# Performance work log

Hardware: AMD Instinct MI355X
Metric: run time of the kernel (lower is better)

## Reference

```python
import jax, jax.numpy as jnp
import numpy as np
from jax import lax

B, L_ENC, L_DEC = 16, 2048, 1024
ENC_IN, MARK_IN, C_OUT = 7, 4, 7
D_MODEL, N_HEADS, D_FF = 512, 8, 2048
E_LAYERS, D_LAYERS, FACTOR, PRED_LEN = 3, 2, 5, 512


def _pos_embed(L, d):
    pos = np.arange(L, dtype=np.float32)[:, None]
    div = np.exp(np.arange(0, d, 2, dtype=np.float32) * -(np.log(10000.0) / d))
    pe = np.zeros((L, d), np.float32)
    pe[:, 0::2] = np.sin(pos * div)
    pe[:, 1::2] = np.cos(pos * div)
    return jnp.asarray(pe)


def _layer_norm(x, g, b, eps=1e-5):
    m = jnp.mean(x, -1, keepdims=True)
    v = jnp.mean((x - m) ** 2, -1, keepdims=True)
    return (x - m) * lax.rsqrt(v + eps) * g + b


def _circ_conv1d(x, w):
    # x:[B,L,Cin], w:[Cout,Cin,3], circular padding=1 (TokenEmbedding / ConvLayer)
    xp = jnp.concatenate([x[:, -1:], x, x[:, :1]], axis=1)
    y = lax.conv_general_dilated(xp.transpose(0, 2, 1), w, (1,), 'VALID',
                                 dimension_numbers=('NCH', 'OIH', 'NCH'))
    return y.transpose(0, 2, 1)


def _prob_attention(q, k, v, mask_flag, rng):
    # q,k,v: [B,L,H,Dh] -> [B,H,L,Dh]
    q, k, v = (t.transpose(0, 2, 1, 3) for t in (q, k, v))
    Bq, H, Lq, Dh = q.shape
    Lk = k.shape[2]
    U_part = min(FACTOR * int(np.ceil(np.log(Lk))), Lk)  # sampled keys per query
    u = min(FACTOR * int(np.ceil(np.log(Lq))), Lq)       # top queries kept
    idx = jax.random.randint(rng, (Lq, U_part), 0, Lk)
    k_sample = k[:, :, idx, :]                           # [B,H,Lq,U,Dh]
    qk_sample = jnp.einsum('bhld,bhlsd->bhls', q, k_sample)
    M = qk_sample.max(-1) - qk_sample.sum(-1) / Lk       # sparsity measure
    _, m_top = lax.top_k(M, u)                            # [B,H,u]
    q_red = jnp.take_along_axis(q, m_top[..., None], axis=2)
    scores = jnp.einsum('bhud,bhkd->bhuk', q_red, k) / np.sqrt(Dh).astype(np.float32)
    if mask_flag:
        tri = jnp.triu(jnp.ones((Lq, Lk), bool), 1)
        scores = jnp.where(tri[m_top], -jnp.inf, scores)  # ProbMask
        ctx = jnp.cumsum(v, axis=2)                       # masked initial context
    else:
        ctx = jnp.broadcast_to(jnp.mean(v, 2, keepdims=True), (Bq, H, Lq, Dh))
    attn = jax.nn.softmax(scores, -1)
    upd = jnp.einsum('bhuk,bhkd->bhud', attn, v)
    bi = jnp.arange(Bq)[:, None, None]
    hi = jnp.arange(H)[None, :, None]
    ctx = ctx.at[bi, hi, m_top].set(upd)                  # scatter top-u contexts
    return ctx.transpose(0, 2, 1, 3)


def _attn_layer(xq, xkv, w, b, mask_flag, rng):
    Bq, Lq, d = xq.shape
    Dh = d // N_HEADS
    q = (xq @ w[0] + b[0]).reshape(Bq, Lq, N_HEADS, Dh)
    k = (xkv @ w[1] + b[1]).reshape(Bq, -1, N_HEADS, Dh)
    v = (xkv @ w[2] + b[2]).reshape(Bq, -1, N_HEADS, Dh)
    out = _prob_attention(q, k, v, mask_flag, rng).reshape(Bq, Lq, d)
    return out @ w[3] + b[3]


def _ffn(x, w1, b1, w2, b2):
    # Conv1d kernel-size-1 pair == pointwise MLP
    return jax.nn.gelu(x @ w1 + b1, approximate=False) @ w2 + b2


def _distil(x, cw, cb, bg, bb):
    y = _circ_conv1d(x, cw) + cb
    y = y * (bg / np.sqrt(1.0 + 1e-5).astype(np.float32)) + bb  # BN eval (mean0,var1)
    y = jax.nn.elu(y)
    y = y.transpose(0, 2, 1)
    y = lax.reduce_window(y, -jnp.inf, lax.max, (1, 1, 3), (1, 1, 2),
                          [(0, 0), (0, 0), (1, 1)])  # MaxPool1d(k=3,s=2,p=1)
    return y.transpose(0, 2, 1)


def setup_inputs() -> dict:
    key = jax.random.key(0)
    ks = iter(jax.random.split(key, 64))
    rn = lambda shape: jax.random.normal(next(ks), shape, jnp.float32) * 0.02
    return {
        'x_enc': jax.random.normal(next(ks), (B, L_ENC, ENC_IN), jnp.float32),
        'x_mark_enc': jax.random.normal(next(ks), (B, L_ENC, MARK_IN), jnp.float32),
        'x_dec': jax.random.normal(next(ks), (B, L_DEC, ENC_IN), jnp.float32),
        'x_mark_dec': jax.random.normal(next(ks), (B, L_DEC, MARK_IN), jnp.float32),
        'enc_tok_w': rn((D_MODEL, ENC_IN, 3)),
        'enc_mark_w': rn((MARK_IN, D_MODEL)),
        'dec_tok_w': rn((D_MODEL, ENC_IN, 3)),
        'dec_mark_w': rn((MARK_IN, D_MODEL)),
        'enc_attn_w': rn((E_LAYERS, 4, D_MODEL, D_MODEL)),
        'enc_attn_b': jnp.zeros((E_LAYERS, 4, D_MODEL), jnp.float32),
        'enc_ffn1_w': rn((E_LAYERS, D_MODEL, D_FF)),
        'enc_ffn1_b': jnp.zeros((E_LAYERS, D_FF), jnp.float32),
        'enc_ffn2_w': rn((E_LAYERS, D_FF, D_MODEL)),
        'enc_ffn2_b': jnp.zeros((E_LAYERS, D_MODEL), jnp.float32),
        'enc_ln_g': jnp.ones((E_LAYERS, 2, D_MODEL), jnp.float32),
        'enc_ln_b': jnp.zeros((E_LAYERS, 2, D_MODEL), jnp.float32),
        'distil_w': rn((E_LAYERS - 1, D_MODEL, D_MODEL, 3)),
        'distil_b': jnp.zeros((E_LAYERS - 1, D_MODEL), jnp.float32),
        'distil_bn_g': jnp.ones((E_LAYERS - 1, D_MODEL), jnp.float32),
        'distil_bn_b': jnp.zeros((E_LAYERS - 1, D_MODEL), jnp.float32),
        'enc_norm_g': jnp.ones((D_MODEL,), jnp.float32),
        'enc_norm_b': jnp.zeros((D_MODEL,), jnp.float32),
        'dec_self_w': rn((D_LAYERS, 4, D_MODEL, D_MODEL)),
        'dec_self_b': jnp.zeros((D_LAYERS, 4, D_MODEL), jnp.float32),
        'dec_cross_w': rn((D_LAYERS, 4, D_MODEL, D_MODEL)),
        'dec_cross_b': jnp.zeros((D_LAYERS, 4, D_MODEL), jnp.float32),
        'dec_ffn1_w': rn((D_LAYERS, D_MODEL, D_FF)),
        'dec_ffn1_b': jnp.zeros((D_LAYERS, D_FF), jnp.float32),
        'dec_ffn2_w': rn((D_LAYERS, D_FF, D_MODEL)),
        'dec_ffn2_b': jnp.zeros((D_LAYERS, D_MODEL), jnp.float32),
        'dec_ln_g': jnp.ones((D_LAYERS, 3, D_MODEL), jnp.float32),
        'dec_ln_b': jnp.zeros((D_LAYERS, 3, D_MODEL), jnp.float32),
        'dec_norm_g': jnp.ones((D_MODEL,), jnp.float32),
        'dec_norm_b': jnp.zeros((D_MODEL,), jnp.float32),
        'proj_w': rn((D_MODEL, C_OUT)),
        'proj_b': jnp.zeros((C_OUT,), jnp.float32),
    }


def reference(x_enc, x_mark_enc, x_dec, x_mark_dec, enc_tok_w, enc_mark_w,
              dec_tok_w, dec_mark_w, enc_attn_w, enc_attn_b, enc_ffn1_w, enc_ffn1_b,
              enc_ffn2_w, enc_ffn2_b, enc_ln_g, enc_ln_b, distil_w, distil_b,
              distil_bn_g, distil_bn_b, enc_norm_g, enc_norm_b, dec_self_w, dec_self_b,
              dec_cross_w, dec_cross_b, dec_ffn1_w, dec_ffn1_b, dec_ffn2_w, dec_ffn2_b,
              dec_ln_g, dec_ln_b, dec_norm_g, dec_norm_b, proj_w, proj_b):
    base = jax.random.key(42)
    # DataEmbedding: token conv + sinusoid positional + time-feature linear
    x = _circ_conv1d(x_enc, enc_tok_w) + _pos_embed(x_enc.shape[1], D_MODEL)[None] + x_mark_enc @ enc_mark_w
    for l in range(E_LAYERS):
        h = x + _attn_layer(x, x, enc_attn_w[l], enc_attn_b[l], False, jax.random.fold_in(base, l))
        h = _layer_norm(h, enc_ln_g[l, 0], enc_ln_b[l, 0])
        y = _ffn(h, enc_ffn1_w[l], enc_ffn1_b[l], enc_ffn2_w[l], enc_ffn2_b[l])
        x = _layer_norm(h + y, enc_ln_g[l, 1], enc_ln_b[l, 1])
        if l < E_LAYERS - 1:  # distil conv halves the length
            x = _distil(x, distil_w[l], distil_b[l], distil_bn_g[l], distil_bn_b[l])
    enc_out = _layer_norm(x, enc_norm_g, enc_norm_b)
    x = _circ_conv1d(x_dec, dec_tok_w) + _pos_embed(x_dec.shape[1], D_MODEL)[None] + x_mark_dec @ dec_mark_w
    for l in range(D_LAYERS):
        h = x + _attn_layer(x, x, dec_self_w[l], dec_self_b[l], True, jax.random.fold_in(base, 100 + 2 * l))
        h = _layer_norm(h, dec_ln_g[l, 0], dec_ln_b[l, 0])
        h = h + _attn_layer(h, enc_out, dec_cross_w[l], dec_cross_b[l], False, jax.random.fold_in(base, 101 + 2 * l))
        h = _layer_norm(h, dec_ln_g[l, 1], dec_ln_b[l, 1])
        y = _ffn(h, dec_ffn1_w[l], dec_ffn1_b[l], dec_ffn2_w[l], dec_ffn2_b[l])
        x = _layer_norm(h + y, dec_ln_g[l, 2], dec_ln_b[l, 2])
    x = _layer_norm(x, dec_norm_g, dec_norm_b)
    out = x @ proj_w + proj_b
    return out[:, -PRED_LEN:, :]
```

## Files before the change

kernel.cpp:

```cpp
#include <hip/hip_runtime.h>
#include <math.h>
#include <stdint.h>

typedef unsigned int u32;
typedef _Float16 f16;
typedef __attribute__((ext_vector_type(8))) _Float16 f16x8;
typedef __attribute__((ext_vector_type(4))) float f32x4;

__host__ __device__ __forceinline__ u32 rotl32(u32 x, int r) { return (x << r) | (x >> (32 - r)); }
__host__ __device__ __forceinline__ void tf_round(u32& x0, u32& x1, int r) {
  x0 += x1; x1 = rotl32(x1, r); x1 ^= x0;
}
__host__ __device__ __forceinline__ void tf_block(u32 k0, u32 k1, u32 x0, u32 x1, u32& o0, u32& o1) {
  u32 k2 = k0 ^ k1 ^ 0x1BD11BDAu;
  x0 += k0; x1 += k1;
  tf_round(x0,x1,13); tf_round(x0,x1,15); tf_round(x0,x1,26); tf_round(x0,x1,6);
  x0 += k1; x1 += k2 + 1u;
  tf_round(x0,x1,17); tf_round(x0,x1,29); tf_round(x0,x1,16); tf_round(x0,x1,24);
  x0 += k2; x1 += k0 + 2u;
  tf_round(x0,x1,13); tf_round(x0,x1,15); tf_round(x0,x1,26); tf_round(x0,x1,6);
  x0 += k0; x1 += k1 + 3u;
  tf_round(x0,x1,17); tf_round(x0,x1,29); tf_round(x0,x1,16); tf_round(x0,x1,24);
  x0 += k1; x1 += k2 + 4u;
  tf_round(x0,x1,13); tf_round(x0,x1,15); tf_round(x0,x1,26); tf_round(x0,x1,6);
  x0 += k2; x1 += k0 + 5u;
  o0 = x0; o1 = x1;
}

__global__ void k_idx(u32 ka, u32 kb, int n, int mask, int* __restrict__ idx) {
  int i = blockIdx.x * 256 + threadIdx.x;
  if (i >= n) return;
  u32 b1, b2; tf_block(ka, kb, 0u, (u32)i, b1, b2);
  idx[i] = (int)((b1 ^ b2) & (u32)mask);
}

__device__ __forceinline__ void emit_split(float v, f16* __restrict__ oh,
                                           f16* __restrict__ ol, size_t o) {
  f16 h = (f16)v;
  oh[o] = h;
  ol[o] = (f16)((v - (float)h) * 2048.0f);
}
__device__ __forceinline__ float rsplit(const f16* __restrict__ h,
                                        const f16* __restrict__ l, size_t o) {
  return (float)h[o] + (float)l[o] * (1.0f / 2048.0f);
}

__global__ void k_pe(float* __restrict__ pe) {
  int i = blockIdx.x * 256 + threadIdx.x;
  if (i >= 2048 * 512) return;
  int t = i >> 9, o = i & 511;
  float arg = (float)((o >> 1) * 2) * (float)(-(log(10000.0) / 512.0));
  float div = (float)exp((double)arg);
  float ang32 = (float)t * div;
  double ang = (double)ang32;
  pe[i] = (float)((o & 1) ? cos(ang) : sin(ang));
}

__global__ __launch_bounds__(256) void k_embed(
    const float* __restrict__ x, const float* __restrict__ mark,
    const float* __restrict__ tw, const float* __restrict__ mw,
    const float* __restrict__ pe, f16* __restrict__ oh, f16* __restrict__ ol,
    int L, int total) {
  int i = blockIdx.x * 256 + threadIdx.x;
  if (i >= total) return;
  int oo = i & 511;
  int bt = i >> 9;
  int t = bt % L;
  int b = bt / L;
  float acc = pe[(t << 9) + oo];
  #pragma unroll
  for (int k = 0; k < 3; ++k) {
    int st = t + k - 1; if (st < 0) st += L; else if (st >= L) st -= L;
    const float* xr = x + (size_t)(b * L + st) * 7;
    const float* wr = tw + oo * 21 + k;
    #pragma unroll
    for (int ii = 0; ii < 7; ++ii) acc += xr[ii] * wr[ii * 3];
  }
  const float* mr = mark + (size_t)bt * 4;
  #pragma unroll
  for (int m = 0; m < 4; ++m) acc += mr[m] * mw[(m << 9) + oo];
  emit_split(acc, oh, ol, ((size_t)bt << 9) + oo);
}

__global__ __launch_bounds__(256) void k_wsplit(const float* __restrict__ W,
    f16* __restrict__ Wh, f16* __restrict__ Wl, int K, int N) {
  size_t zo = (size_t)blockIdx.z * K * N;
  W += zo; Wh += zo; Wl += zo;
  __shared__ float tile[32][33];
  int kb = blockIdx.x << 5, nb = blockIdx.y << 5;
  int t = threadIdx.x;
  int tr = t >> 5, tc = t & 31;
  #pragma unroll
  for (int p = 0; p < 4; ++p)
    tile[tr + p * 8][tc] = W[(size_t)(kb + tr + p * 8) * N + nb + tc];
  __syncthreads();
  #pragma unroll
  for (int p = 0; p < 4; ++p) {
    int n = tr + p * 8, k = tc;
    float v = tile[k][n];
    f16 h = (f16)v;
    size_t o = (size_t)(nb + n) * K + kb + k;
    Wh[o] = h;
    Wl[o] = (f16)((v - (float)h) * 2048.0f);
  }
}

__global__ void k_wsplit_conv(const float* __restrict__ w, f16* __restrict__ Wh, f16* __restrict__ Wl) {
  int i = blockIdx.x * 256 + threadIdx.x;
  if (i >= 512 * 1536) return;
  int o = i / 1536, k = i - o * 1536;
  float v = w[(size_t)o * 1536 + (k & 511) * 3 + (k >> 9)];
  f16 h = (f16)v;
  Wh[i] = h;
  Wl[i] = (f16)((v - (float)h) * 2048.0f);
}

__device__ __forceinline__ int swz_x(int r) { return ((((r >> 1) & 3) ^ ((r >> 3) & 3)) << 4); }

__device__ __forceinline__ void gload16(const void* g, void* l) {
  __builtin_amdgcn_global_load_lds(
      (const __attribute__((address_space(1))) void*)g,
      (__attribute__((address_space(3))) void*)l, 16, 0, 0);
}

template<int ACT, int OSPLIT, int GATHER, int RESID>
__global__ __launch_bounds__(256, 2) void k_mgemm2(
    const f16* __restrict__ Ah, const f16* __restrict__ Al,
    const f16* __restrict__ Bh, const f16* __restrict__ Bl,
    const float* __restrict__ bias,
    const f16* __restrict__ Rh, const f16* __restrict__ Rl,
    const float* __restrict__ bns, const float* __restrict__ bnb,
    float* __restrict__ C, f16* __restrict__ Ch, f16* __restrict__ Cl,
    int M, int N, int K, int lgL) {
  __shared__ char lds[65536];
  const int t = threadIdx.x;
  int nwg = gridDim.x * gridDim.y;
  int bid = blockIdx.y * gridDim.x + blockIdx.x;
  if ((nwg & 7) == 0) {
    int cpx = nwg >> 3;
    bid = (bid & 7) * cpx + (bid >> 3);
  }
  const int bm = (bid / gridDim.x) << 7, bn = (bid % gridDim.x) << 7;
  const int w = t >> 6, l = t & 63;
  const int lr = l >> 2;
  const int qx = (l & 3) << 4;
  const int wr = (w >> 1) << 6, wc = (w & 1) << 6;
  const int fr = l & 15;
  const int fkB = (l >> 4) << 4;
  const f32x4 zero = {0.f, 0.f, 0.f, 0.f};
  f32x4 acc1[4][4], acc2[4][4];
  #pragma unroll
  for (int i = 0; i < 4; ++i)
    #pragma unroll
    for (int j = 0; j < 4; ++j) { acc1[i][j] = zero; acc2[i][j] = zero; }

  auto stage = [&](int k0, int bufo) {
    #pragma unroll
    for (int c = 0; c < 2; ++c) {
      int r = w * 32 + c * 16 + lr;
      int sx = qx ^ swz_x(r);
      const char *gAh, *gAl;
      if (GATHER) {
        int m = bm + r;
        int Lm = 1 << lgL;
        int ab = m >> lgL, at = m & (Lm - 1);
        int ke = k0 + (sx >> 1);
        int tap = ke >> 9, ii = ke & 511;
        int st = at + tap - 1; if (st < 0) st += Lm; else if (st >= Lm) st -= Lm;
        size_t aoff = (((size_t)((ab << lgL) + st)) << 9) + ii;
        gAh = (const char*)(Ah + aoff);
        gAl = (const char*)(Al + aoff);
      } else {
        gAh = (const char*)(Ah + (size_t)(bm + r) * K + k0) + sx;
        gAl = (const char*)(Al + (size_t)(bm + r) * K + k0) + sx;
      }
      const char* gBh = (const char*)(Bh + (size_t)(bn + r) * K + k0) + sx;
      const char* gBl = (const char*)(Bl + (size_t)(bn + r) * K + k0) + sx;
      char* base = lds + bufo + w * 2048 + c * 1024;
      gload16(gAh, base);
      gload16(gAl, base + 8192);
      gload16(gBh, base + 16384);
      gload16(gBl, base + 24576);
    }
  };

  int nt = K >> 5;
  stage(0, 0);
  __syncthreads();
  int bufo = 0;
  for (int tt = 0; tt < nt; ++tt) {
    int nb = bufo ^ 32768;
    if (tt + 1 < nt) stage((tt + 1) << 5, nb);
    char* pAh = lds + bufo;
    char* pAl = pAh + 8192;
    char* pBh = pAh + 16384;
    char* pBl = pAh + 24576;
    f16x8 ah4[4], al4[4];
    #pragma unroll
    for (int i = 0; i < 4; ++i) {
      int r = wr + i * 16 + fr;
      int ob = r * 64 + (fkB ^ swz_x(r));
      ah4[i] = *(f16x8*)(pAh + ob);
      al4[i] = *(f16x8*)(pAl + ob);
    }
    #pragma unroll
    for (int j = 0; j < 4; ++j) {
      int r = wc + j * 16 + fr;
      int ob = r * 64 + (fkB ^ swz_x(r));
      f16x8 bh_ = *(f16x8*)(pBh + ob);
      f16x8 bl_ = *(f16x8*)(pBl + ob);
      #pragma unroll
      for (int i = 0; i < 4; ++i) {
        acc1[i][j] = __builtin_amdgcn_mfma_f32_16x16x32_f16(ah4[i], bh_, acc1[i][j], 0, 0, 0);
        acc2[i][j] = __builtin_amdgcn_mfma_f32_16x16x32_f16(ah4[i], bl_, acc2[i][j], 0, 0, 0);
        acc2[i][j] = __builtin_amdgcn_mfma_f32_16x16x32_f16(al4[i], bh_, acc2[i][j], 0, 0, 0);
      }
    }
    __syncthreads();
    bufo = nb;
  }
  #pragma unroll
  for (int j = 0; j < 4; ++j) {
    int col = bn + wc + j * 16 + fr;
    float bsv = bias[col];
    float g2 = 0.f, b2 = 0.f;
    if (ACT == 2) { g2 = bns[col] * 0.9999950000375f; b2 = bnb[col]; }
    #pragma unroll
    for (int i = 0; i < 4; ++i) {
      #pragma unroll
      for (int r = 0; r < 4; ++r) {
        int row = bm + wr + i * 16 + ((l >> 4) << 2) + r;
        float v = acc1[i][j][r] + acc2[i][j][r] * (1.0f / 2048.0f) + bsv;
        if (ACT == 1) v = 0.5f * v * (1.0f + erff(v * 0.70710678118654752f));
        if (ACT == 2) { v = v * g2 + b2; v = v > 0.f ? v : expm1f(v); }
        size_t oi = (size_t)row * N + col;
        if (RESID) v += rsplit(Rh, Rl, oi);
        if (OSPLIT) emit_split(v, Ch, Cl, oi);
        else        C[oi] = v;
      }
    }
  }
}

__global__ __launch_bounds__(256) void k_ln(const f16* __restrict__ xh, const f16* __restrict__ xl,
    const float* __restrict__ g, const float* __restrict__ b,
    float* __restrict__ of32, f16* __restrict__ oh, f16* __restrict__ ol) {
  int row = blockIdx.x, t = threadIdx.x;
  size_t base = (size_t)row << 9;
  float v0 = rsplit(xh, xl, base + t);
  float v1 = rsplit(xh, xl, base + t + 256);
  float s = v0 + v1;
  #pragma unroll
  for (int off = 32; off; off >>= 1) s += __shfl_down(s, off);
  __shared__ float ls[4];
  if ((t & 63) == 0) ls[t >> 6] = s;
  __syncthreads();
  float mean = (ls[0] + ls[1] + ls[2] + ls[3]) * (1.f / 512.f);
  __syncthreads();
  float d0 = v0 - mean, d1 = v1 - mean;
  float q = d0 * d0 + d1 * d1;
  #pragma unroll
  for (int off = 32; off; off >>= 1) q += __shfl_down(q, off);
  if ((t & 63) == 0) ls[t >> 6] = q;
  __syncthreads();
  float var = (ls[0] + ls[1] + ls[2] + ls[3]) * (1.f / 512.f);
  float rs = rsqrtf(var + 1e-5f);
  float r0 = d0 * rs * g[t] + b[t];
  float r1 = d1 * rs * g[t + 256] + b[t + 256];
  if (of32) { of32[base + t] = r0; of32[base + t + 256] = r1; }
  if (oh) {
    emit_split(r0, oh, ol, base + t);
    emit_split(r1, oh, ol, base + t + 256);
  }
}

__global__ __launch_bounds__(256) void k_qkM(const float* __restrict__ Q, int qstr,
    const float* __restrict__ Kp, int kstr, const int* __restrict__ idx,
    float* __restrict__ M, int Lq, int Lk, int U) {
  __shared__ float qsh[4][2][64];
  __shared__ int idxs[4][2][40];
  int nwg = gridDim.x;
  int bid = blockIdx.x;
  if ((nwg & 7) == 0) {
    int cpx = nwg >> 3;
    bid = (bid & 7) * cpx + (bid >> 3);
  }
  int wib = threadIdx.x >> 6;
  int wid = (bid << 2) + wib;
  int lane = threadIdx.x & 63;
  int Lh = Lq >> 1;
  int lp = wid & (Lh - 1);
  int bh = wid / Lh;
  int l0 = lp * 2;
  int h = bh & 7; int b = bh >> 3;
  if (lane < 32) {
    int q = lane >> 4, e = lane & 15;
    const float4* qr = (const float4*)(Q + (size_t)(b * Lq + l0 + q) * qstr + (h << 6));
    *(float4*)(&qsh[wib][q][e * 4]) = qr[e];
  }
  if (lane < U) {
    idxs[wib][0][lane] = idx[l0 * U + lane];
    idxs[wib][1][lane] = idx[(l0 + 1) * U + lane];
  }
  __syncthreads();
  int g = lane >> 2, j = lane & 3;
  float mx0 = -INFINITY, sm0 = 0.f, mx1 = -INFINITY, sm1 = 0.f;
  #pragma unroll
  for (int p = 0; p < 5; ++p) {
    int sp = p * 16 + g;
    int q = (sp >= U) ? 1 : 0;
    int s = sp - U * q;
    bool act = sp < 2 * U;
    int kr = idxs[wib][act ? q : 0][act ? s : 0];
    const float* kb_ = Kp + (size_t)((size_t)b * Lk + kr) * kstr + (h << 6);
    float4 c0 = *(const float4*)(kb_ +  0 + 4 * j);
    float4 c1 = *(const float4*)(kb_ + 16 + 4 * j);
    float4 c2 = *(const float4*)(kb_ + 32 + 4 * j);
    float4 c3 = *(const float4*)(kb_ + 48 + 4 * j);
    const float* qs = qsh[wib][act ? q : 0];
    float pd = 0.f;
    pd += qs[ 0 + 4*j] * c0.x + qs[ 1 + 4*j] * c0.y + qs[ 2 + 4*j] * c0.z + qs[ 3 + 4*j] * c0.w;
    pd += qs[16 + 4*j] * c1.x + qs[17 + 4*j] * c1.y + qs[18 + 4*j] * c1.z + qs[19 + 4*j] * c1.w;
    pd += qs[32 + 4*j] * c2.x + qs[33 + 4*j] * c2.y + qs[34 + 4*j] * c2.z + qs[35 + 4*j] * c2.w;
    pd += qs[48 + 4*j] * c3.x + qs[49 + 4*j] * c3.y + qs[50 + 4*j] * c3.z + qs[51 + 4*j] * c3.w;
    pd += __shfl_xor(pd, 1);
    pd += __shfl_xor(pd, 2);
    if (act) {
      if (q == 0) { mx0 = fmaxf(mx0, pd); sm0 += pd; }
      else        { mx1 = fmaxf(mx1, pd); sm1 += pd; }
    }
  }
  #pragma unroll
  for (int off = 32; off >= 4; off >>= 1) {
    mx0 = fmaxf(mx0, __shfl_xor(mx0, off)); sm0 += __shfl_xor(sm0, off);
    mx1 = fmaxf(mx1, __shfl_xor(mx1, off)); sm1 += __shfl_xor(sm1, off);
  }
  if (lane == 0) {
    M[(size_t)bh * Lq + l0]     = mx0 - sm0 / (float)Lk;
    M[(size_t)bh * Lq + l0 + 1] = mx1 - sm1 / (float)Lk;
  }
}

__global__ void k_topk64(const float* __restrict__ M, int* __restrict__ mtop, int Lq, int u) {
  __shared__ float vals[2048];
  int bh = blockIdx.x, l = threadIdx.x;
  const float* Mr = M + (size_t)bh * Lq;
  for (int i = l; i < Lq; i += 64) vals[i] = Mr[i];
  __syncthreads();
  for (int it = 0; it < u; ++it) {
    float bv = -INFINITY; int bi = 0x7fffffff;
    for (int i = l; i < Lq; i += 64) {
      float v = vals[i];
      if (v > bv || (v == bv && i < bi)) { bv = v; bi = i; }
    }
    #pragma unroll
    for (int off = 32; off; off >>= 1) {
      float vv = __shfl_xor(bv, off); int ii = __shfl_xor(bi, off);
      if (vv > bv || (vv == bv && ii < bi)) { bv = vv; bi = ii; }
    }
    if (l == 0) { mtop[bh * u + it] = bi; vals[bi] = -INFINITY; }
    __syncthreads();
  }
}

__global__ void k_cm1(const float* __restrict__ V, int vstr, float* __restrict__ PS,
                      int Lk, int rows) {
  int bid = blockIdx.x;
  int bh = bid >> 4, seg = bid & 15, d = threadIdx.x;
  int b = bh >> 3, h = bh & 7;
  const float* vp = V + (size_t)(b * Lk + seg * rows) * vstr + (h << 6) + d;
  float acc = 0.f;
  for (int r = 0; r < rows; ++r) acc += vp[(size_t)r * vstr];
  PS[(bid << 6) + d] = acc;
}
__global__ void k_cm2(const float* __restrict__ PS, f16* __restrict__ AOh,
                      f16* __restrict__ AOl, float invLk, int Lq, int total) {
  int i = blockIdx.x * 256 + threadIdx.x;
  if (i >= total) return;
  int c = i & 511; int h = c >> 6; int d = c & 63;
  int r = i >> 9; int b = r / Lq;
  float acc = 0.f;
  #pragma unroll
  for (int s = 0; s < 16; ++s) acc += PS[(((((b << 3) + h) << 4) + s) << 6) + d];
  emit_split(acc * invLk, AOh, AOl, (size_t)i);
}

__global__ void k_cs1(const float* __restrict__ V, int vstr, float* __restrict__ PS,
                      int Lq, int rows) {
  int bid = blockIdx.x;
  int bh = bid >> 3, seg = bid & 7, d = threadIdx.x;
  int b = bh >> 3, h = bh & 7;
  const float* vp = V + (size_t)(b * Lq + seg * rows) * vstr + (h << 6) + d;
  float acc = 0.f;
  for (int r = 0; r < rows; ++r) acc += vp[(size_t)r * vstr];
  PS[(bid << 6) + d] = acc;
}
__global__ void k_cs3(const float* __restrict__ V, int vstr, const float* __restrict__ PS,
                      f16* __restrict__ AOh, f16* __restrict__ AOl, int Lq, int rows) {
  int bid = blockIdx.x;
  int bh = bid >> 3, seg = bid & 7, d = threadIdx.x;
  int b = bh >> 3, h = bh & 7;
  float acc = 0.f;
  for (int s2 = 0; s2 < seg; ++s2) acc += PS[(((bh << 3) + s2) << 6) + d];
  const float* vp = V + (size_t)(b * Lq + seg * rows) * vstr + (h << 6) + d;
  size_t ob = ((size_t)(b * Lq + seg * rows) << 9) + (h << 6) + d;
  for (int r = 0; r < rows; ++r) {
    acc += vp[(size_t)r * vstr];
    emit_split(acc, AOh, AOl, ob + ((size_t)r << 9));
  }
}

__global__ __launch_bounds__(256) void k_sattnF(
    const float* __restrict__ Q, int qstr, const float* __restrict__ Kp, int kstr,
    const float* __restrict__ Vp, int vstr, const int* __restrict__ mtop,
    float* __restrict__ PPm, float* __restrict__ PPs, float* __restrict__ PPv,
    int Lq, int Lk, int u, int masked, int bhn, int chunk) {
  __shared__ float Qs[40 * 64];
  __shared__ float Kt[64 * 65];
  __shared__ float Vs[64 * 65];
  __shared__ float els[40 * 64];
  __shared__ int rowsh[40];
  int ch = blockIdx.x, bh = blockIdx.y;
  int b = bh >> 3, h = bh & 7;
  int c0 = ch * chunk;
  int nkt = chunk >> 6;
  int t = threadIdx.x;
  int g = t >> 6, d = t & 63;
  if (t < 40) rowsh[t] = (t < u) ? mtop[bh * u + t] : -1;
  __syncthreads();
  for (int i = t; i < 40 * 16; i += 256) {
    int r = i >> 4, e4 = i & 15;
    int row = rowsh[r];
    float4 v;
    if (row >= 0) v = *(const float4*)(Q + (size_t)(b * Lq + row) * qstr + (h << 6) + e4 * 4);
    else          v = make_float4(0.f, 0.f, 0.f, 0.f);
    *(float4*)(Qs + r * 64 + e4 * 4) = v;
  }
  int rows_[10];
  __syncthreads();
  #pragma unroll
  for (int i = 0; i < 10; ++i) rows_[i] = rowsh[g + i * 4];
  float pv[10], m[10], sum[10];
  #pragma unroll
  for (int i = 0; i < 10; ++i) { pv[i] = 0.f; m[i] = -INFINITY; sum[i] = 0.f; }
  const int srow = t >> 2, seg = t & 3;
  for (int kt = 0; kt < nkt; ++kt) {
    __syncthreads();
    {
      int crow = c0 + (kt << 6) + srow;
      const float* kp2 = Kp + (size_t)(b * Lk + crow) * kstr + (h << 6) + seg * 16;
      const float* vp2 = Vp + (size_t)(b * Lk + crow) * vstr + (h << 6) + seg * 16;
      #pragma unroll
      for (int q4 = 0; q4 < 4; ++q4) {
        float4 kv = *(const float4*)(kp2 + q4 * 4);
        float4 vv = *(const float4*)(vp2 + q4 * 4);
        int e0 = seg * 16 + q4 * 4;
        Kt[(e0 + 0) * 65 + srow] = kv.x;
        Kt[(e0 + 1) * 65 + srow] = kv.y;
        Kt[(e0 + 2) * 65 + srow] = kv.z;
        Kt[(e0 + 3) * 65 + srow] = kv.w;
        Vs[srow * 65 + e0 + 0] = vv.x;
        Vs[srow * 65 + e0 + 1] = vv.y;
        Vs[srow * 65 + e0 + 2] = vv.z;
        Vs[srow * 65 + e0 + 3] = vv.w;
      }
    }
    __syncthreads();
    float dot[10];
    #pragma unroll
    for (int i = 0; i < 10; ++i) dot[i] = 0.f;
    for (int e = 0; e < 64; ++e) {
      float kv = Kt[e * 65 + d];
      #pragma unroll
      for (int i = 0; i < 10; ++i)
        dot[i] += Qs[(g + i * 4) * 64 + e] * kv;
    }
    int key = c0 + (kt << 6) + d;
    float scale_[10];
    #pragma unroll
    for (int i = 0; i < 10; ++i) {
      float s = dot[i] * 0.125f;
      if (masked && key > rows_[i]) s = -INFINITY;
      float tm = s;
      #pragma unroll
      for (int off = 32; off; off >>= 1) tm = fmaxf(tm, __shfl_xor(tm, off));
      float nm = fmaxf(m[i], tm);
      if (nm > -3e38f) {
        float scl = expf(m[i] - nm);
        float e_ = expf(s - nm);
        float ts = e_;
        #pragma unroll
        for (int off = 32; off; off >>= 1) ts += __shfl_xor(ts, off);
        sum[i] = sum[i] * scl + ts;
        m[i] = nm;
        scale_[i] = scl;
        els[(g + i * 4) * 64 + d] = e_;
      } else {
        scale_[i] = 1.f;
        els[(g + i * 4) * 64 + d] = 0.f;
      }
    }
    __syncthreads();
    float acc[10];
    #pragma unroll
    for (int i = 0; i < 10; ++i) acc[i] = 0.f;
    for (int k = 0; k < 64; ++k) {
      float vv = Vs[k * 65 + d];
      #pragma unroll
      for (int i = 0; i < 10; ++i)
        acc[i] += els[(g + i * 4) * 64 + k] * vv;
    }
    #pragma unroll
    for (int i = 0; i < 10; ++i) pv[i] = pv[i] * scale_[i] + acc[i];
  }
  #pragma unroll
  for (int i = 0; i < 10; ++i) {
    int r = g + i * 4;
    if (r < u) {
      size_t pidx = (size_t)(ch * bhn + bh) * u + r;
      if (d == 0) { PPm[pidx] = m[i]; PPs[pidx] = sum[i]; }
      PPv[pidx * 64 + d] = pv[i];
    }
  }
}

__global__ void k_sattnc(const float* __restrict__ PPm, const float* __restrict__ PPs,
                         const float* __restrict__ PPv, const int* __restrict__ mtop,
                         f16* __restrict__ AOh, f16* __restrict__ AOl,
                         int Lq, int u, int nch, int bhn) {
  int rowid = blockIdx.x;
  int bh = rowid / u, ui = rowid % u;
  int d = threadIdx.x;
  int b = bh >> 3, h = bh & 7;
  int row = mtop[bh * u + ui];
  float M = -INFINITY;
  for (int c = 0; c < nch; ++c)
    M = fmaxf(M, PPm[(size_t)(c * bhn + bh) * u + ui]);
  float S = 0.f, o = 0.f;
  for (int c = 0; c < nch; ++c) {
    size_t pidx = (size_t)(c * bhn + bh) * u + ui;
    float pm = PPm[pidx];
    float sc = (pm > -3e38f) ? expf(pm - M) : 0.f;
    S += sc * PPs[pidx];
    o += sc * PPv[pidx * 64 + d];
  }
  emit_split(o / S, AOh, AOl, ((size_t)(b * Lq + row) << 9) + (h << 6) + d);
}

__global__ void k_maxpool(const float* __restrict__ y, f16* __restrict__ oh,
                          f16* __restrict__ ol, int L) {
  int Lo = L >> 1;
  int i = blockIdx.x * 256 + threadIdx.x;
  int c = i & 511; int bj = i >> 9;
  int j = bj % Lo; int b = bj / Lo;
  float m = -INFINITY;
  int t0 = 2 * j - 1;
  #pragma unroll
  for (int k = 0; k < 3; ++k) {
    int tt = t0 + k;
    if (tt >= 0 && tt < L) m = fmaxf(m, y[((size_t)(b * L + tt) << 9) + c]);
  }
  emit_split(m, oh, ol, ((size_t)(b * Lo + j) << 9) + c);
}

__global__ void k_proj(const float* __restrict__ Xn, const float* __restrict__ pw,
                       const float* __restrict__ pb, float* __restrict__ out) {
  int i = blockIdx.x * 256 + threadIdx.x;
  if (i >= 16 * 512 * 7) return;
  int c = i % 7; int r = i / 7;
  int b = r >> 9; int j = r & 511;
  const float* xr = Xn + ((size_t)(b * 1024 + 512 + j) << 9);
  float acc = pb[c];
  for (int d2 = 0; d2 < 512; ++d2) acc += xr[d2] * pw[d2 * 7 + c];
  out[i] = acc;
}

extern "C" void kernel_launch(void* const* d_in, const int* in_sizes, int n_in,
                              void* d_out, int out_size, void* d_ws, size_t ws_size,
                              hipStream_t stream) {
  const float* x_enc      = (const float*)d_in[0];
  const float* x_mark_enc = (const float*)d_in[1];
  const float* x_dec      = (const float*)d_in[2];
  const float* x_mark_dec = (const float*)d_in[3];
  const float* enc_tok_w  = (const float*)d_in[4];
  const float* enc_mark_w = (const float*)d_in[5];
  const float* dec_tok_w  = (const float*)d_in[6];
  const float* dec_mark_w = (const float*)d_in[7];
  const float* enc_attn_w = (const float*)d_in[8];
  const float* enc_attn_b = (const float*)d_in[9];
  const float* enc_ffn1_w = (const float*)d_in[10];
  const float* enc_ffn1_b = (const float*)d_in[11];
  const float* enc_ffn2_w = (const float*)d_in[12];
  const float* enc_ffn2_b = (const float*)d_in[13];
  const float* enc_ln_g   = (const float*)d_in[14];
  const float* enc_ln_b   = (const float*)d_in[15];
  const float* distil_w   = (const float*)d_in[16];
  const float* distil_b   = (const float*)d_in[17];
  const float* distil_bn_g= (const float*)d_in[18];
  const float* distil_bn_b= (const float*)d_in[19];
  const float* enc_norm_g = (const float*)d_in[20];
  const float* enc_norm_b = (const float*)d_in[21];
  const float* dec_self_w = (const float*)d_in[22];
  const float* dec_self_b = (const float*)d_in[23];
  const float* dec_cross_w= (const float*)d_in[24];
  const float* dec_cross_b= (const float*)d_in[25];
  const float* dec_ffn1_w = (const float*)d_in[26];
  const float* dec_ffn1_b = (const float*)d_in[27];
  const float* dec_ffn2_w = (const float*)d_in[28];
  const float* dec_ffn2_b = (const float*)d_in[29];
  const float* dec_ln_g   = (const float*)d_in[30];
  const float* dec_ln_b   = (const float*)d_in[31];
  const float* dec_norm_g = (const float*)d_in[32];
  const float* dec_norm_b = (const float*)d_in[33];
  const float* proj_w     = (const float*)d_in[34];
  const float* proj_b     = (const float*)d_in[35];

  float* ws = (float*)d_ws;
  size_t off = 0;
  f16* Xh   = (f16*)(ws + off); off += 16777216;
  f16* Xl   = Xh + 16777216;
  f16* ENCh = (f16*)(ws + off); off += 4194304;
  f16* ENCl = ENCh + 4194304;
  float* PE = ws + off; off += 1048576;
  float* Mb = ws + off; off += 131072;
  float* PS = ws + off; off += 65536;
  f16* WSP  = (f16*)(ws + off); off += 2097152;
  int* IDXi = (int*)(ws + off); off += 84480;
  float* Y  = ws + off;
  int* MTi  = IDXi + 81920;
  size_t need4 = (off + 16777216ull) * 4;
  size_t need8 = (off + 33554432ull) * 4;
  int bs;
  if      (ws_size >= need8) bs = 8;
  else if (ws_size >= need4) bs = 4;
  else return;
  f16* Yh = (f16*)Y;
  f16* Yl = Yh + 16777216;
  float* WF  = (float*)WSP + 1048576;
  float* PPm = WF;
  float* PPs = WF + 16384;
  float* PPv = WF + 32768;

  auto ln = [&](const f16* xh, const f16* xl, const float* g, const float* b, int rows,
                float* of32, f16* oh, f16* ol) {
    k_ln<<<rows, 256, 0, stream>>>(xh, xl, g, b, of32, oh, ol);
  };
  auto wsplit = [&](const float* W, f16* Wh, f16* Wl, int K, int N, int nmat) {
    dim3 g(K >> 5, N >> 5, nmat);
    k_wsplit<<<g, 256, 0, stream>>>(W, Wh, Wl, K, N);
  };
  auto mgQ = [&](const f16* Ah, const f16* Al, const f16* Wh, const f16* Wl,
                 const float* bias, float* C, int M, int N, int K) {
    dim3 g(N >> 7, M >> 7);
    k_mgemm2<0,0,0,0><<<g, 256, 0, stream>>>(Ah, Al, Wh, Wl, bias, nullptr, nullptr,
        nullptr, nullptr, C, nullptr, nullptr, M, N, K, 0);
  };
  auto mgR = [&](const f16* Ah, const f16* Al, const f16* Wh, const f16* Wl,
                 const float* bias, const f16* Rh, const f16* Rl,
                 f16* Ch, f16* Cl, int M, int N, int K) {
    dim3 g(N >> 7, M >> 7);
    k_mgemm2<0,1,0,1><<<g, 256, 0, stream>>>(Ah, Al, Wh, Wl, bias, Rh, Rl,
        nullptr, nullptr, nullptr, Ch, Cl, M, N, K, 0);
  };
  auto mgG = [&](const f16* Ah, const f16* Al, const f16* Wh, const f16* Wl,
                 const float* bias, f16* Ch, f16* Cl, int M, int N, int K) {
    dim3 g(N >> 7, M >> 7);
    k_mgemm2<1,1,0,0><<<g, 256, 0, stream>>>(Ah, Al, Wh, Wl, bias, nullptr, nullptr,
        nullptr, nullptr, nullptr, Ch, Cl, M, N, K, 0);
  };
  auto Uof = [](int Lx) { int v = 5 * (int)ceil(log((double)Lx)); return v < Lx ? v : Lx; };

  auto attn = [&](f16* xqh, f16* xql, const f16* xkvh, const f16* xkvl,
                  int Lq, int Lk, const float* w, const float* bias,
                  bool masked, u32 fold, bool selfa) {
    int U = Uof(Lk), uu = Uof(Lq);
    u32 r0, r1, ka, kb2;
    tf_block(0u, 42u, 0u, fold, r0, r1);
    tf_block(r0, r1, 0u, 1u, ka, kb2);
    int n = Lq * U;
    k_idx<<<(n + 255) / 256, 256, 0, stream>>>(ka, kb2, n, Lk - 1, IDXi);

    f16 *Wqkvh = WSP,            *Wqkvl = WSP + 786432;
    f16 *WQh   = WSP,            *WQl   = WSP + 262144;
    f16 *WKVh  = WSP + 524288,   *WKVl  = WSP + 1048576;
    f16 *WOh   = WSP + 1572864,  *WOl   = WSP + 1835008;
    if (selfa) {
      wsplit(w, Wqkvh, Wqkvl, 512, 512, 3);
    } else {
      wsplit(w, WQh, WQl, 512, 512, 1);
      wsplit(w + 262144, WKVh, WKVl, 512, 512, 2);
    }
    wsplit(w + 786432, WOh, WOl, 512, 512, 1);

    int nsl = 16 / bs;
    int bhn = bs * 8;
    for (int s = 0; s < nsl; ++s) {
      size_t qoff = (size_t)s * bs * Lq * 512;
      size_t koff = (size_t)s * bs * Lk * 512;
      const float *qp, *kp, *vp;
      int qstr, kstr, vstr;
      f16 *AOh, *AOl;
      if (selfa) {
        float* QKV = Y;
        AOh = (f16*)(Y + (size_t)bs * Lq * 1536);
        AOl = AOh + (size_t)bs * Lq * 512;
        mgQ(xqh + qoff, xql + qoff, Wqkvh, Wqkvl, bias, QKV, bs * Lq, 1536, 512);
        qp = QKV; qstr = 1536; kp = QKV + 512; kstr = 1536; vp = QKV + 1024; vstr = 1536;
      } else {
        float* Qb  = Y;
        float* KVb = Y + (size_t)bs * Lq * 512;
        AOh = (f16*)(KVb + (size_t)bs * Lk * 1024);
        AOl = AOh + (size_t)bs * Lq * 512;
        mgQ(xqh + qoff, xql + qoff, WQh, WQl, bias, Qb, bs * Lq, 512, 512);
        mgQ(xkvh + koff, xkvl + koff, WKVh, WKVl, bias + 512, KVb, bs * Lk, 1024, 512);
        qp = Qb; qstr = 512; kp = KVb; kstr = 1024; vp = KVb + 512; vstr = 1024;
      }
      int wids = bhn * Lq;
      k_qkM<<<wids / 8, 256, 0, stream>>>(qp, qstr, kp, kstr, IDXi, Mb, Lq, Lk, U);
      k_topk64<<<bhn, 64, 0, stream>>>(Mb, MTi, Lq, uu);
      if (masked) {
        k_cs1<<<bhn * 8, 64, 0, stream>>>(vp, vstr, PS, Lq, Lq >> 3);
        k_cs3<<<bhn * 8, 64, 0, stream>>>(vp, vstr, PS, AOh, AOl, Lq, Lq >> 3);
      } else {
        k_cm1<<<bhn * 16, 64, 0, stream>>>(vp, vstr, PS, Lk, Lk >> 4);
        int tot = bs * Lq * 512;
        k_cm2<<<tot / 256, 256, 0, stream>>>(PS, AOh, AOl, 1.0f / (float)Lk, Lq, tot);
      }
      int chunk = (Lk >= 2048) ? 512 : ((Lk >= 1024) ? 256 : 128);
      int nch = Lk / chunk;
      dim3 gs(nch, bhn);
      k_sattnF<<<gs, 256, 0, stream>>>(qp, qstr, kp, kstr, vp, vstr, MTi,
                                       PPm, PPs, PPv, Lq, Lk, uu, masked ? 1 : 0, bhn, chunk);
      k_sattnc<<<bhn * uu, 64, 0, stream>>>(PPm, PPs, PPv, MTi, AOh, AOl, Lq, uu, nch, bhn);
      mgR(AOh, AOl, WOh, WOl, bias + 1536, xqh + qoff, xql + qoff,
          xqh + qoff, xql + qoff, bs * Lq, 512, 512);
    }
  };

  auto ffn = [&](f16* xh, f16* xl, const float* w1, const float* b1,
                 const float* w2, const float* b2, int Mtot) {
    f16 *W1h = WSP,           *W1l = WSP + 1048576,
        *W2h = WSP + 2097152, *W2l = WSP + 3145728;
    wsplit(w1, W1h, W1l, 512, 2048, 1);
    wsplit(w2, W2h, W2l, 2048, 512, 1);
    for (int c0 = 0; c0 < Mtot; c0 += 8192) {
      int rows = (Mtot - c0 < 8192) ? (Mtot - c0) : 8192;
      mgG(xh + (size_t)c0 * 512, xl + (size_t)c0 * 512, W1h, W1l, b1, Yh, Yl, rows, 2048, 512);
      mgR(Yh, Yl, W2h, W2l, b2, xh + (size_t)c0 * 512, xl + (size_t)c0 * 512,
          xh + (size_t)c0 * 512, xl + (size_t)c0 * 512, rows, 512, 2048);
    }
  };

  k_pe<<<(2048 * 512) / 256, 256, 0, stream>>>(PE);
  k_embed<<<(16 * 2048 * 512) / 256, 256, 0, stream>>>(x_enc, x_mark_enc, enc_tok_w, enc_mark_w,
                                                       PE, Xh, Xl, 2048, 16 * 2048 * 512);
  int L = 2048;
  for (int l = 0; l < 3; ++l) {
    attn(Xh, Xl, Xh, Xl, L, L, enc_attn_w + (size_t)l * 4 * 262144,
         enc_attn_b + (size_t)l * 2048, false, (u32)l, true);
    ln(Xh, Xl, enc_ln_g + (size_t)(l * 2) * 512, enc_ln_b + (size_t)(l * 2) * 512, 16 * L,
       nullptr, Xh, Xl);
    ffn(Xh, Xl, enc_ffn1_w + (size_t)l * 512 * 2048, enc_ffn1_b + (size_t)l * 2048,
        enc_ffn2_w + (size_t)l * 2048 * 512, enc_ffn2_b + (size_t)l * 512, 16 * L);
    ln(Xh, Xl, enc_ln_g + (size_t)(l * 2 + 1) * 512, enc_ln_b + (size_t)(l * 2 + 1) * 512, 16 * L,
       nullptr, Xh, Xl);
    if (l < 2) {
      f16 *Dh = WSP, *Dl = WSP + 786432;
      k_wsplit_conv<<<(512 * 1536) / 256, 256, 0, stream>>>(distil_w + (size_t)l * 512 * 512 * 3, Dh, Dl);
      dim3 g(512 >> 7, (16 * L) >> 7);
      int lgL = (L == 2048) ? 11 : 10;
      k_mgemm2<2,0,1,0><<<g, 256, 0, stream>>>(Xh, Xl, Dh, Dl, distil_b + (size_t)l * 512,
          nullptr, nullptr, distil_bn_g + (size_t)l * 512, distil_bn_b + (size_t)l * 512,
          Y, nullptr, nullptr, 16 * L, 512, 1536, lgL);
      int Lo = L >> 1;
      k_maxpool<<<(16 * Lo * 512) / 256, 256, 0, stream>>>(Y, Xh, Xl, L);
      L = Lo;
    }
  }
  ln(Xh, Xl, enc_norm_g, enc_norm_b, 16 * 512, nullptr, ENCh, ENCl);

  k_embed<<<(16 * 1024 * 512) / 256, 256, 0, stream>>>(x_dec, x_mark_dec, dec_tok_w, dec_mark_w,
                                                       PE, Xh, Xl, 1024, 16 * 1024 * 512);
  for (int l = 0; l < 2; ++l) {
    attn(Xh, Xl, Xh, Xl, 1024, 1024, dec_self_w + (size_t)l * 4 * 262144,
         dec_self_b + (size_t)l * 2048, true, (u32)(100 + 2 * l), true);
    ln(Xh, Xl, dec_ln_g + (size_t)(l * 3) * 512, dec_ln_b + (size_t)(l * 3) * 512, 16384,
       nullptr, Xh, Xl);
    attn(Xh, Xl, ENCh, ENCl, 1024, 512, dec_cross_w + (size_t)l * 4 * 262144,
         dec_cross_b + (size_t)l * 2048, false, (u32)(101 + 2 * l), false);
    ln(Xh, Xl, dec_ln_g + (size_t)(l * 3 + 1) * 512, dec_ln_b + (size_t)(l * 3 + 1) * 512, 16384,
       nullptr, Xh, Xl);
    ffn(Xh, Xl, dec_ffn1_w + (size_t)l * 512 * 2048, dec_ffn1_b + (size_t)l * 2048,
        dec_ffn2_w + (size_t)l * 2048 * 512, dec_ffn2_b + (size_t)l * 512, 16384);
    ln(Xh, Xl, dec_ln_g + (size_t)(l * 3 + 2) * 512, dec_ln_b + (size_t)(l * 3 + 2) * 512, 16384,
       nullptr, Xh, Xl);
  }
  ln(Xh, Xl, dec_norm_g, dec_norm_b, 16384, Y, nullptr, nullptr);
  k_proj<<<(16 * 512 * 7 + 255) / 256, 256, 0, stream>>>(Y, proj_w, proj_b, (float*)d_out);
}
```

Measured before the change: 6.163 ms.

## Process four queries per wave in qkM, widen cumsum split, merge weight splits, larger FFN chunk

The sparsity-measure kernel now has each wavefront handle four query rows instead of two, which halves the grid and reuses the index and Q staging. The masked cumulative-sum kernels split each head into 16 segments instead of 8 for more parallelism. The four attention weight splits are merged into a single wsplit launch. The FFN row chunk doubles to 16384 when the batch slice is 8, to cut launch count. The trade-offs are a dynamic loop with more branching in qkM and a larger FFN intermediate buffer that must fit in the workspace.

```diff
diff --git a/kernel.cpp b/kernel.cpp
--- a/kernel.cpp
+++ b/kernel.cpp
@@ -277,8 +277,8 @@
 __global__ __launch_bounds__(256) void k_qkM(const float* __restrict__ Q, int qstr,
     const float* __restrict__ Kp, int kstr, const int* __restrict__ idx,
     float* __restrict__ M, int Lq, int Lk, int U) {
-  __shared__ float qsh[4][2][64];
-  __shared__ int idxs[4][2][40];
+  __shared__ float qsh[4][4][64];
+  __shared__ int idxs[4][4][40];
   int nwg = gridDim.x;
   int bid = blockIdx.x;
   if ((nwg & 7) == 0) {
@@ -288,36 +288,38 @@
   int wib = threadIdx.x >> 6;
   int wid = (bid << 2) + wib;
   int lane = threadIdx.x & 63;
-  int Lh = Lq >> 1;
+  int Lh = Lq >> 2;
   int lp = wid & (Lh - 1);
   int bh = wid / Lh;
-  int l0 = lp * 2;
+  int l0 = lp * 4;
   int h = bh & 7; int b = bh >> 3;
-  if (lane < 32) {
+  {
     int q = lane >> 4, e = lane & 15;
     const float4* qr = (const float4*)(Q + (size_t)(b * Lq + l0 + q) * qstr + (h << 6));
     *(float4*)(&qsh[wib][q][e * 4]) = qr[e];
   }
   if (lane < U) {
-    idxs[wib][0][lane] = idx[l0 * U + lane];
-    idxs[wib][1][lane] = idx[(l0 + 1) * U + lane];
+    #pragma unroll
+    for (int q = 0; q < 4; ++q)
+      idxs[wib][q][lane] = idx[(l0 + q) * U + lane];
   }
   __syncthreads();
   int g = lane >> 2, j = lane & 3;
   float mx0 = -INFINITY, sm0 = 0.f, mx1 = -INFINITY, sm1 = 0.f;
-  #pragma unroll
-  for (int p = 0; p < 5; ++p) {
+  float mx2 = -INFINITY, sm2 = 0.f, mx3 = -INFINITY, sm3 = 0.f;
+  int npass = (4 * U + 15) >> 4;
+  for (int p = 0; p < npass; ++p) {
     int sp = p * 16 + g;
-    int q = (sp >= U) ? 1 : 0;
-    int s = sp - U * q;
-    bool act = sp < 2 * U;
-    int kr = idxs[wib][act ? q : 0][act ? s : 0];
+    bool act = sp < 4 * U;
+    int q = act ? sp / U : 0;
+    int s = act ? sp - q * U : 0;
+    int kr = idxs[wib][q][s];
     const float* kb_ = Kp + (size_t)((size_t)b * Lk + kr) * kstr + (h << 6);
     float4 c0 = *(const float4*)(kb_ +  0 + 4 * j);
     float4 c1 = *(const float4*)(kb_ + 16 + 4 * j);
     float4 c2 = *(const float4*)(kb_ + 32 + 4 * j);
     float4 c3 = *(const float4*)(kb_ + 48 + 4 * j);
-    const float* qs = qsh[wib][act ? q : 0];
+    const float* qs = qsh[wib][q];
     float pd = 0.f;
     pd += qs[ 0 + 4*j] * c0.x + qs[ 1 + 4*j] * c0.y + qs[ 2 + 4*j] * c0.z + qs[ 3 + 4*j] * c0.w;
     pd += qs[16 + 4*j] * c1.x + qs[17 + 4*j] * c1.y + qs[18 + 4*j] * c1.z + qs[19 + 4*j] * c1.w;
@@ -326,18 +328,24 @@
     pd += __shfl_xor(pd, 1);
     pd += __shfl_xor(pd, 2);
     if (act) {
-      if (q == 0) { mx0 = fmaxf(mx0, pd); sm0 += pd; }
-      else        { mx1 = fmaxf(mx1, pd); sm1 += pd; }
+      if (q == 0)      { mx0 = fmaxf(mx0, pd); sm0 += pd; }
+      else if (q == 1) { mx1 = fmaxf(mx1, pd); sm1 += pd; }
+      else if (q == 2) { mx2 = fmaxf(mx2, pd); sm2 += pd; }
+      else             { mx3 = fmaxf(mx3, pd); sm3 += pd; }
     }
   }
   #pragma unroll
   for (int off = 32; off >= 4; off >>= 1) {
     mx0 = fmaxf(mx0, __shfl_xor(mx0, off)); sm0 += __shfl_xor(sm0, off);
     mx1 = fmaxf(mx1, __shfl_xor(mx1, off)); sm1 += __shfl_xor(sm1, off);
+    mx2 = fmaxf(mx2, __shfl_xor(mx2, off)); sm2 += __shfl_xor(sm2, off);
+    mx3 = fmaxf(mx3, __shfl_xor(mx3, off)); sm3 += __shfl_xor(sm3, off);
   }
   if (lane == 0) {
     M[(size_t)bh * Lq + l0]     = mx0 - sm0 / (float)Lk;
     M[(size_t)bh * Lq + l0 + 1] = mx1 - sm1 / (float)Lk;
+    M[(size_t)bh * Lq + l0 + 2] = mx2 - sm2 / (float)Lk;
+    M[(size_t)bh * Lq + l0 + 3] = mx3 - sm3 / (float)Lk;
   }
 }
 
@@ -388,7 +396,7 @@
 __global__ void k_cs1(const float* __restrict__ V, int vstr, float* __restrict__ PS,
                       int Lq, int rows) {
   int bid = blockIdx.x;
-  int bh = bid >> 3, seg = bid & 7, d = threadIdx.x;
+  int bh = bid >> 4, seg = bid & 15, d = threadIdx.x;
   int b = bh >> 3, h = bh & 7;
   const float* vp = V + (size_t)(b * Lq + seg * rows) * vstr + (h << 6) + d;
   float acc = 0.f;
@@ -398,10 +406,10 @@
 __global__ void k_cs3(const float* __restrict__ V, int vstr, const float* __restrict__ PS,
                       f16* __restrict__ AOh, f16* __restrict__ AOl, int Lq, int rows) {
   int bid = blockIdx.x;
-  int bh = bid >> 3, seg = bid & 7, d = threadIdx.x;
+  int bh = bid >> 4, seg = bid & 15, d = threadIdx.x;
   int b = bh >> 3, h = bh & 7;
   float acc = 0.f;
-  for (int s2 = 0; s2 < seg; ++s2) acc += PS[(((bh << 3) + s2) << 6) + d];
+  for (int s2 = 0; s2 < seg; ++s2) acc += PS[(((bh << 4) + s2) << 6) + d];
   const float* vp = V + (size_t)(b * Lq + seg * rows) * vstr + (h << 6) + d;
   size_t ob = ((size_t)(b * Lq + seg * rows) << 9) + (h << 6) + d;
   for (int r = 0; r < rows; ++r) {
@@ -635,7 +643,6 @@
   else if (ws_size >= need4) bs = 4;
   else return;
   f16* Yh = (f16*)Y;
-  f16* Yl = Yh + 16777216;
   float* WF  = (float*)WSP + 1048576;
   float* PPm = WF;
   float* PPs = WF + 16384;
@@ -680,17 +687,12 @@
     int n = Lq * U;
     k_idx<<<(n + 255) / 256, 256, 0, stream>>>(ka, kb2, n, Lk - 1, IDXi);
 
-    f16 *Wqkvh = WSP,            *Wqkvl = WSP + 786432;
-    f16 *WQh   = WSP,            *WQl   = WSP + 262144;
-    f16 *WKVh  = WSP + 524288,   *WKVl  = WSP + 1048576;
-    f16 *WOh   = WSP + 1572864,  *WOl   = WSP + 1835008;
-    if (selfa) {
-      wsplit(w, Wqkvh, Wqkvl, 512, 512, 3);
-    } else {
-      wsplit(w, WQh, WQl, 512, 512, 1);
-      wsplit(w + 262144, WKVh, WKVl, 512, 512, 2);
-    }
-    wsplit(w + 786432, WOh, WOl, 512, 512, 1);
+    f16 *Wh = WSP, *Wl = WSP + 1048576;
+    wsplit(w, Wh, Wl, 512, 512, 4);
+    f16 *Wqkvh = Wh,           *Wqkvl = Wl;
+    f16 *WQh   = Wh,           *WQl   = Wl;
+    f16 *WKVh  = Wh + 262144,  *WKVl  = Wl + 262144;
+    f16 *WOh   = Wh + 786432,  *WOl   = Wl + 786432;
 
     int nsl = 16 / bs;
     int bhn = bs * 8;
@@ -716,11 +718,11 @@
         qp = Qb; qstr = 512; kp = KVb; kstr = 1024; vp = KVb + 512; vstr = 1024;
       }
       int wids = bhn * Lq;
-      k_qkM<<<wids / 8, 256, 0, stream>>>(qp, qstr, kp, kstr, IDXi, Mb, Lq, Lk, U);
+      k_qkM<<<wids / 16, 256, 0, stream>>>(qp, qstr, kp, kstr, IDXi, Mb, Lq, Lk, U);
       k_topk64<<<bhn, 64, 0, stream>>>(Mb, MTi, Lq, uu);
       if (masked) {
-        k_cs1<<<bhn * 8, 64, 0, stream>>>(vp, vstr, PS, Lq, Lq >> 3);
-        k_cs3<<<bhn * 8, 64, 0, stream>>>(vp, vstr, PS, AOh, AOl, Lq, Lq >> 3);
+        k_cs1<<<bhn * 16, 64, 0, stream>>>(vp, vstr, PS, Lq, Lq >> 4);
+        k_cs3<<<bhn * 16, 64, 0, stream>>>(vp, vstr, PS, AOh, AOl, Lq, Lq >> 4);
       } else {
         k_cm1<<<bhn * 16, 64, 0, stream>>>(vp, vstr, PS, Lk, Lk >> 4);
         int tot = bs * Lq * 512;
@@ -743,10 +745,12 @@
         *W2h = WSP + 2097152, *W2l = WSP + 3145728;
     wsplit(w1, W1h, W1l, 512, 2048, 1);
     wsplit(w2, W2h, W2l, 2048, 512, 1);
-    for (int c0 = 0; c0 < Mtot; c0 += 8192) {
-      int rows = (Mtot - c0 < 8192) ? (Mtot - c0) : 8192;
-      mgG(xh + (size_t)c0 * 512, xl + (size_t)c0 * 512, W1h, W1l, b1, Yh, Yl, rows, 2048, 512);
-      mgR(Yh, Yl, W2h, W2l, b2, xh + (size_t)c0 * 512, xl + (size_t)c0 * 512,
+    int chunk = (bs == 8) ? 16384 : 8192;
+    f16* Yl2 = Yh + (size_t)chunk * 2048;
+    for (int c0 = 0; c0 < Mtot; c0 += chunk) {
+      int rows = (Mtot - c0 < chunk) ? (Mtot - c0) : chunk;
+      mgG(xh + (size_t)c0 * 512, xl + (size_t)c0 * 512, W1h, W1l, b1, Yh, Yl2, rows, 2048, 512);
+      mgR(Yh, Yl2, W2h, W2l, b2, xh + (size_t)c0 * 512, xl + (size_t)c0 * 512,
           xh + (size_t)c0 * 512, xl + (size_t)c0 * 512, rows, 512, 2048);
     }
   };
```

Result: faster. 5.839 ms (-5.3%).
